# Optimization experiments

Measured on AMD Instinct MI355X. Metric: run time of the kernel, lower is better.

The kernel has to match this reference:

```python
import jax, jax.numpy as jnp
import numpy as np

B, H = 65536, 512


def setup_inputs() -> dict:
    key = jax.random.key(0)
    ks = jax.random.split(key, 10)
    s = 1.0 / np.sqrt(H)  # torch nn.Linear default init range
    uni = lambda k, shape: jax.random.uniform(k, shape, jnp.float32, -s, s)
    return {
        "inputs": jax.random.normal(ks[0], (B, H), jnp.float32),
        "short_term_memory": jax.random.normal(ks[1], (B, H), jnp.float32),
        "Wf": uni(ks[2], (H, H)), "bf": uni(ks[3], (H,)),
        "Wi": uni(ks[4], (H, H)), "bi": uni(ks[5], (H,)),
        "Wg": uni(ks[6], (H, H)), "bg": uni(ks[7], (H,)),
        "Wo": uni(ks[8], (H, H)), "bo": uni(ks[9], (H,)),
    }


def reference(inputs, short_term_memory, Wf, bf, Wi, bi, Wg, bg, Wo, bo):
    z = inputs + short_term_memory  # [B, H]
    # ForgetGate: OVERWRITES long-term memory (previous cell state never read).
    c = jax.nn.sigmoid(z @ Wf.T + bf)
    # InputGate: c += sigmoid(...) * tanh(...)
    c = c + jax.nn.sigmoid(z @ Wi.T + bi) * jnp.tanh(z @ Wg.T + bg)
    # OutputGate: h = tanh(c) * sigmoid(...)
    h = jnp.tanh(c) * jax.nn.sigmoid(z @ Wo.T + bo)
    return jnp.stack((c, h))  # [2, B, H]: new long-term and short-term memory
```

## Files before the change

### kernel.cpp

```cpp
#include <hip/hip_runtime.h>

typedef __bf16 bf16x8 __attribute__((ext_vector_type(8)));
typedef float  f32x4  __attribute__((ext_vector_type(4)));

#define LOG2E 1.4426950408889634f

static __device__ __forceinline__ float fexp2(float x) { return __builtin_amdgcn_exp2f(x); }
static __device__ __forceinline__ float frcp(float x)  { return __builtin_amdgcn_rcpf(x); }
static __device__ __forceinline__ float fsigmoid(float x) { return frcp(1.0f + fexp2(-LOG2E * x)); }
static __device__ __forceinline__ float ftanh(float x)    { return 2.0f * frcp(1.0f + fexp2(-2.0f * LOG2E * x)) - 1.0f; }

__global__ __launch_bounds__(256) void wpack(const float* __restrict__ Wf,
                                             const float* __restrict__ Wi,
                                             const float* __restrict__ Wg,
                                             const float* __restrict__ Wo,
                                             __bf16* __restrict__ Wp)
{
    int idx = blockIdx.x * 256 + threadIdx.x;
    int kg  = idx & 63;
    int j   = (idx >> 6) & 511;
    int g   = idx >> 15;
    const float* src = (g == 0) ? Wf : (g == 1) ? Wi : (g == 2) ? Wg : Wo;
    const float4* s4 = (const float4*)(src + j * 512 + kg * 8);
    float4 v0 = s4[0], v1 = s4[1];
    bf16x8 o;
    o[0] = (__bf16)v0.x; o[1] = (__bf16)v0.y; o[2] = (__bf16)v0.z; o[3] = (__bf16)v0.w;
    o[4] = (__bf16)v1.x; o[5] = (__bf16)v1.y; o[6] = (__bf16)v1.z; o[7] = (__bf16)v1.w;
    int cn = j >> 4;
    int ks = kg >> 2;
    int lt = (j & 15) + (kg & 3) * 16;
    size_t dst = ((size_t)(((g * 32 + cn) * 16 + ks) * 64 + lt)) * 8;
    *(bf16x8*)(Wp + dst) = o;
}

__global__ __launch_bounds__(1024, 4) void lstm_main(
    const float* __restrict__ xin, const float* __restrict__ stm,
    const __bf16* __restrict__ Wp,
    const float* __restrict__ bfv, const float* __restrict__ biv,
    const float* __restrict__ bgv, const float* __restrict__ bov,
    float* __restrict__ out)
{
    __shared__ unsigned char zs[131072];
    const int tid  = threadIdx.x;
    const int lane = tid & 63;
    const int wv   = tid >> 6;
    const int cn8  = wv & 7;
    const int rh   = wv >> 3;
    const int l15  = lane & 15;
    const int lq   = lane >> 4;
    const int row0 = blockIdx.x * 128;

    {
        const float* xb = xin + (size_t)row0 * 512;
        const float* sb = stm + (size_t)row0 * 512;
        #pragma unroll
        for (int it = 0; it < 8; ++it) {
            int idx = it * 1024 + tid;
            int row = idx >> 6;
            int kg  = idx & 63;
            const float4* x4 = (const float4*)(xb + row * 512 + kg * 8);
            const float4* s4 = (const float4*)(sb + row * 512 + kg * 8);
            float4 a0 = x4[0], a1 = x4[1];
            float4 b0 = s4[0], b1 = s4[1];
            bf16x8 p;
            p[0] = (__bf16)(a0.x + b0.x); p[1] = (__bf16)(a0.y + b0.y);
            p[2] = (__bf16)(a0.z + b0.z); p[3] = (__bf16)(a0.w + b0.w);
            p[4] = (__bf16)(a1.x + b1.x); p[5] = (__bf16)(a1.y + b1.y);
            p[6] = (__bf16)(a1.z + b1.z); p[7] = (__bf16)(a1.w + b1.w);
            int rb   = row >> 5;
            int kk   = kg >> 1;
            int slot = ((row & 31) + (kg & 1) * 32) ^ (kk & 7);
            *(bf16x8*)(zs + rb * 32768 + kk * 1024 + slot * 16) = p;
        }
    }
    __syncthreads();

    const int kkoff = lq >> 1;
    const int s0    = l15 + (lq & 1) * 32;
    const int koffb = kkoff << 10;
    const int abase = rh * 65536;

    for (int ci = 0; ci < 4; ++ci) {
        const int cn   = ci * 8 + cn8;
        const int colj = cn * 16 + l15;

        const __bf16* bp0 = Wp + ((size_t)((  0 + cn) * 16)) * 512 + lane * 8;
        const __bf16* bp1 = Wp + ((size_t)(( 32 + cn) * 16)) * 512 + lane * 8;
        const __bf16* bp2 = Wp + ((size_t)(( 64 + cn) * 16)) * 512 + lane * 8;
        const __bf16* bp3 = Wp + ((size_t)(( 96 + cn) * 16)) * 512 + lane * 8;

        float bias0 = bfv[colj], bias1 = biv[colj], bias2 = bgv[colj], bias3 = bov[colj];
        f32x4 acc[4][4];
        #pragma unroll
        for (int m = 0; m < 4; ++m) {
            #pragma unroll
            for (int r = 0; r < 4; ++r) {
                acc[m][0][r] = bias0; acc[m][1][r] = bias1;
                acc[m][2][r] = bias2; acc[m][3][r] = bias3;
            }
        }

        #pragma unroll 2
        for (int ks = 0; ks < 16; ++ks) {
            const int kk7 = ((2 * ks) & 7) | kkoff;
            const int t0  = abase + ((s0 ^ kk7) << 4) + ks * 2048 + koffb;
            bf16x8 b0 = *(const bf16x8*)(bp0 + ks * 512);
            bf16x8 b1 = *(const bf16x8*)(bp1 + ks * 512);
            bf16x8 b2 = *(const bf16x8*)(bp2 + ks * 512);
            bf16x8 b3 = *(const bf16x8*)(bp3 + ks * 512);
            bf16x8 a[4];
            #pragma unroll
            for (int m = 0; m < 4; ++m)
                a[m] = *(const bf16x8*)(zs + (m >> 1) * 32768 + (m & 1) * 256 + t0);
            #pragma unroll
            for (int m = 0; m < 4; ++m) {
                acc[m][0] = __builtin_amdgcn_mfma_f32_16x16x32_bf16(a[m], b0, acc[m][0], 0, 0, 0);
                acc[m][1] = __builtin_amdgcn_mfma_f32_16x16x32_bf16(a[m], b1, acc[m][1], 0, 0, 0);
                acc[m][2] = __builtin_amdgcn_mfma_f32_16x16x32_bf16(a[m], b2, acc[m][2], 0, 0, 0);
                acc[m][3] = __builtin_amdgcn_mfma_f32_16x16x32_bf16(a[m], b3, acc[m][3], 0, 0, 0);
            }
        }

        #pragma unroll
        for (int m = 0; m < 4; ++m) {
            #pragma unroll
            for (int r = 0; r < 4; ++r) {
                float F = acc[m][0][r], I = acc[m][1][r];
                float G = acc[m][2][r], O = acc[m][3][r];
                float c = fsigmoid(F) + fsigmoid(I) * ftanh(G);
                float h = ftanh(c) * fsigmoid(O);
                int row = row0 + rh * 64 + m * 16 + lq * 4 + r;
                int o   = row * 512 + colj;
                out[o] = c;
                out[33554432 + o] = h;
            }
        }
    }
}

extern "C" void kernel_launch(void* const* d_in, const int* in_sizes, int n_in,
                              void* d_out, int out_size, void* d_ws, size_t ws_size,
                              hipStream_t stream) {
    const float* xin = (const float*)d_in[0];
    const float* stm = (const float*)d_in[1];
    const float* Wf  = (const float*)d_in[2];
    const float* bf_ = (const float*)d_in[3];
    const float* Wi  = (const float*)d_in[4];
    const float* bi_ = (const float*)d_in[5];
    const float* Wg  = (const float*)d_in[6];
    const float* bg_ = (const float*)d_in[7];
    const float* Wo  = (const float*)d_in[8];
    const float* bo_ = (const float*)d_in[9];
    __bf16* Wp = (__bf16*)d_ws;

    wpack<<<512, 256, 0, stream>>>(Wf, Wi, Wg, Wo, Wp);
    lstm_main<<<512, 1024, 0, stream>>>(xin, stm, Wp, bf_, bi_, bg_, bo_, (float*)d_out);
}
```

Measured before the change: 202.7 us.

## Split gates across wave halves and exchange accumulators through LDS

Each wave now computes two gates for all 128 rows of the block instead of all four gates for 64 rows. Each weight fragment loaded from global memory is therefore reused across 8 row tiles rather than 4, halving B-operand traffic per wave. The cost is doubled A-operand LDS reads per wave, a 32 KB LDS exchange buffer, and extra __syncthreads in the epilogue to swap partial gate results between the paired waves. The larger LDS footprint may also lower occupancy.

```diff
diff --git a/kernel.cpp b/kernel.cpp
--- a/kernel.cpp
+++ b/kernel.cpp
@@ -41,6 +41,7 @@
     float* __restrict__ out)
 {
     __shared__ unsigned char zs[131072];
+    __shared__ unsigned char xbuf[32768];
     const int tid  = threadIdx.x;
     const int lane = tid & 63;
     const int wv   = tid >> 6;
@@ -78,58 +79,66 @@
     const int kkoff = lq >> 1;
     const int s0    = l15 + (lq & 1) * 32;
     const int koffb = kkoff << 10;
-    const int abase = rh * 65536;
+
+    const float* bias_a = rh ? bgv : bfv;
+    const float* bias_b = rh ? bov : biv;
 
     for (int ci = 0; ci < 4; ++ci) {
         const int cn   = ci * 8 + cn8;
         const int colj = cn * 16 + l15;
 
-        const __bf16* bp0 = Wp + ((size_t)((  0 + cn) * 16)) * 512 + lane * 8;
-        const __bf16* bp1 = Wp + ((size_t)(( 32 + cn) * 16)) * 512 + lane * 8;
-        const __bf16* bp2 = Wp + ((size_t)(( 64 + cn) * 16)) * 512 + lane * 8;
-        const __bf16* bp3 = Wp + ((size_t)(( 96 + cn) * 16)) * 512 + lane * 8;
+        const __bf16* bpA = Wp + ((size_t)(((rh * 2    ) * 32 + cn) * 16)) * 512 + lane * 8;
+        const __bf16* bpB = Wp + ((size_t)(((rh * 2 + 1) * 32 + cn) * 16)) * 512 + lane * 8;
 
-        float bias0 = bfv[colj], bias1 = biv[colj], bias2 = bgv[colj], bias3 = bov[colj];
-        f32x4 acc[4][4];
+        float biasA = bias_a[colj], biasB = bias_b[colj];
+        f32x4 acc[8][2];
         #pragma unroll
-        for (int m = 0; m < 4; ++m) {
+        for (int m = 0; m < 8; ++m) {
             #pragma unroll
-            for (int r = 0; r < 4; ++r) {
-                acc[m][0][r] = bias0; acc[m][1][r] = bias1;
-                acc[m][2][r] = bias2; acc[m][3][r] = bias3;
-            }
+            for (int r = 0; r < 4; ++r) { acc[m][0][r] = biasA; acc[m][1][r] = biasB; }
         }
 
         #pragma unroll 2
         for (int ks = 0; ks < 16; ++ks) {
             const int kk7 = ((2 * ks) & 7) | kkoff;
-            const int t0  = abase + ((s0 ^ kk7) << 4) + ks * 2048 + koffb;
-            bf16x8 b0 = *(const bf16x8*)(bp0 + ks * 512);
-            bf16x8 b1 = *(const bf16x8*)(bp1 + ks * 512);
-            bf16x8 b2 = *(const bf16x8*)(bp2 + ks * 512);
-            bf16x8 b3 = *(const bf16x8*)(bp3 + ks * 512);
-            bf16x8 a[4];
+            const int t0  = ((s0 ^ kk7) << 4) + ks * 2048 + koffb;
+            bf16x8 b0 = *(const bf16x8*)(bpA + ks * 512);
+            bf16x8 b1 = *(const bf16x8*)(bpB + ks * 512);
+            bf16x8 a[8];
             #pragma unroll
-            for (int m = 0; m < 4; ++m)
+            for (int m = 0; m < 8; ++m)
                 a[m] = *(const bf16x8*)(zs + (m >> 1) * 32768 + (m & 1) * 256 + t0);
             #pragma unroll
-            for (int m = 0; m < 4; ++m) {
+            for (int m = 0; m < 8; ++m) {
                 acc[m][0] = __builtin_amdgcn_mfma_f32_16x16x32_bf16(a[m], b0, acc[m][0], 0, 0, 0);
                 acc[m][1] = __builtin_amdgcn_mfma_f32_16x16x32_bf16(a[m], b1, acc[m][1], 0, 0, 0);
-                acc[m][2] = __builtin_amdgcn_mfma_f32_16x16x32_bf16(a[m], b2, acc[m][2], 0, 0, 0);
-                acc[m][3] = __builtin_amdgcn_mfma_f32_16x16x32_bf16(a[m], b3, acc[m][3], 0, 0, 0);
             }
         }
 
+        unsigned char* wr = xbuf + ((cn8 * 2 + rh) * 2) * 1024 + lane * 16;
+        unsigned char* rd = xbuf + ((cn8 * 2 + (1 - rh)) * 2) * 1024 + lane * 16;
         #pragma unroll
-        for (int m = 0; m < 4; ++m) {
+        for (int mc = 0; mc < 4; ++mc) {
+            __syncthreads();
+            if (rh == 0) {
+                *(f32x4*)(wr)        = acc[mc + 4][0];
+                *(f32x4*)(wr + 1024) = acc[mc + 4][1];
+            } else {
+                *(f32x4*)(wr)        = acc[mc][0];
+                *(f32x4*)(wr + 1024) = acc[mc][1];
+            }
+            __syncthreads();
+            f32x4 t0v = *(const f32x4*)(rd);
+            f32x4 t1v = *(const f32x4*)(rd + 1024);
+            int mo = rh ? (mc + 4) : mc;
             #pragma unroll
             for (int r = 0; r < 4; ++r) {
-                float F = acc[m][0][r], I = acc[m][1][r];
-                float G = acc[m][2][r], O = acc[m][3][r];
+                float F, I, G, O;
+                if (rh == 0) { F = acc[mc][0][r];     I = acc[mc][1][r];     G = t0v[r]; O = t1v[r]; }
+                else         { F = t0v[r]; I = t1v[r]; G = acc[mc + 4][0][r]; O = acc[mc + 4][1][r]; }
                 float c = fsigmoid(F) + fsigmoid(I) * ftanh(G);
                 float h = ftanh(c) * fsigmoid(O);
-                int row = row0 + rh * 64 + m * 16 + lq * 4 + r;
+                int row = row0 + mo * 16 + lq * 4 + r;
                 int o   = row * 512 + colj;
                 out[o] = c;
                 out[33554432 + o] = h;
```

New measurement: 219.8 us. 1.08x slower.

## Make LSTM kernel persistent with double-buffered z tiles and gate-interleaved weights

Applied to the files above, without the earlier changes.

The main kernel becomes persistent: 256 blocks of 512 threads each process four 64-row tiles. While MFMAs run on the current tile, the next tile's inputs are loaded and summed into a second LDS buffer. Weights are repacked so the four gates for a k-step sit next to each other, letting one base pointer fetch all four B fragments. This aims to hide global-load latency behind compute, at the cost of fewer waves per CU, more register pressure from the prefetch registers, and a grid that no longer matches a one-block-per-tile launch.

```diff
diff --git a/kernel.cpp b/kernel.cpp
--- a/kernel.cpp
+++ b/kernel.cpp
@@ -29,11 +29,11 @@
     int cn = j >> 4;
     int ks = kg >> 2;
     int lt = (j & 15) + (kg & 3) * 16;
-    size_t dst = ((size_t)(((g * 32 + cn) * 16 + ks) * 64 + lt)) * 8;
+    size_t dst = ((size_t)(((cn * 16 + ks) * 4 + g) * 64 + lt)) * 8;
     *(bf16x8*)(Wp + dst) = o;
 }
 
-__global__ __launch_bounds__(1024, 4) void lstm_main(
+__global__ __launch_bounds__(512, 2) void lstm_main(
     const float* __restrict__ xin, const float* __restrict__ stm,
     const __bf16* __restrict__ Wp,
     const float* __restrict__ bfv, const float* __restrict__ biv,
@@ -44,98 +44,125 @@
     const int tid  = threadIdx.x;
     const int lane = tid & 63;
     const int wv   = tid >> 6;
-    const int cn8  = wv & 7;
-    const int rh   = wv >> 3;
     const int l15  = lane & 15;
     const int lq   = lane >> 4;
-    const int row0 = blockIdx.x * 128;
+    const int b    = blockIdx.x;
+
+    const int kkoff = lq >> 1;
+    const int sl0   = l15 + (lq & 1) * 32;
+    const int koffb = kkoff << 10;
+
+    const int st_kk   = lane >> 1;
+    const int st_hi   = (lane & 1) << 5;
+    const int st_xor  = st_kk & 7;
+    const int st_base = st_kk << 10;
+
+#define STLOAD(X0, X1, S0, S1, RND, ROWB) { \
+    const float* xp_ = xin + ((ROWB) + (RND) * 8 + wv) * 512 + lane * 8; \
+    const float* sp_ = stm + ((ROWB) + (RND) * 8 + wv) * 512 + lane * 8; \
+    X0 = *(const float4*)(xp_);     X1 = *(const float4*)(xp_ + 4); \
+    S0 = *(const float4*)(sp_);     S1 = *(const float4*)(sp_ + 4); }
+
+#define STWRITE(X0, X1, S0, S1, RND, BUF) { \
+    bf16x8 p_; \
+    p_[0] = (__bf16)(X0.x + S0.x); p_[1] = (__bf16)(X0.y + S0.y); \
+    p_[2] = (__bf16)(X0.z + S0.z); p_[3] = (__bf16)(X0.w + S0.w); \
+    p_[4] = (__bf16)(X1.x + S1.x); p_[5] = (__bf16)(X1.y + S1.y); \
+    p_[6] = (__bf16)(X1.z + S1.z); p_[7] = (__bf16)(X1.w + S1.w); \
+    int row_ = (RND) * 8 + wv; \
+    int byte_ = ((row_ >> 5) << 15) | st_base | \
+                (((((row_ & 31) + st_hi)) ^ st_xor) << 4); \
+    *(bf16x8*)((BUF) + byte_) = p_; }
+
+    unsigned char* bufc = zs;
+    unsigned char* bufn = zs + 65536;
 
     {
-        const float* xb = xin + (size_t)row0 * 512;
-        const float* sb = stm + (size_t)row0 * 512;
+        const size_t prow = (size_t)b * 64;
         #pragma unroll
-        for (int it = 0; it < 8; ++it) {
-            int idx = it * 1024 + tid;
-            int row = idx >> 6;
-            int kg  = idx & 63;
-            const float4* x4 = (const float4*)(xb + row * 512 + kg * 8);
-            const float4* s4 = (const float4*)(sb + row * 512 + kg * 8);
-            float4 a0 = x4[0], a1 = x4[1];
-            float4 b0 = s4[0], b1 = s4[1];
-            bf16x8 p;
-            p[0] = (__bf16)(a0.x + b0.x); p[1] = (__bf16)(a0.y + b0.y);
-            p[2] = (__bf16)(a0.z + b0.z); p[3] = (__bf16)(a0.w + b0.w);
-            p[4] = (__bf16)(a1.x + b1.x); p[5] = (__bf16)(a1.y + b1.y);
-            p[6] = (__bf16)(a1.z + b1.z); p[7] = (__bf16)(a1.w + b1.w);
-            int rb   = row >> 5;
-            int kk   = kg >> 1;
-            int slot = ((row & 31) + (kg & 1) * 32) ^ (kk & 7);
-            *(bf16x8*)(zs + rb * 32768 + kk * 1024 + slot * 16) = p;
+        for (int rnd = 0; rnd < 8; ++rnd) {
+            float4 x0, x1, s0v, s1v;
+            STLOAD(x0, x1, s0v, s1v, rnd, prow)
+            STWRITE(x0, x1, s0v, s1v, rnd, bufc)
         }
     }
     __syncthreads();
 
-    const int kkoff = lq >> 1;
-    const int s0    = l15 + (lq & 1) * 32;
-    const int koffb = kkoff << 10;
-    const int abase = rh * 65536;
+    for (int t = 0; t < 4; ++t) {
+        const int tile = b + t * 256;
+        const int row0 = tile * 64;
+        const bool stg = (t < 3);
+        const size_t nrow = (size_t)(tile + 256) * 64;
 
-    for (int ci = 0; ci < 4; ++ci) {
-        const int cn   = ci * 8 + cn8;
-        const int colj = cn * 16 + l15;
+        for (int ci = 0; ci < 4; ++ci) {
+            const int cn   = ci * 8 + wv;
+            const int colj = cn * 16 + l15;
+            const __bf16* bp = Wp + (size_t)cn * 32768 + lane * 8;
 
-        const __bf16* bp0 = Wp + ((size_t)((  0 + cn) * 16)) * 512 + lane * 8;
-        const __bf16* bp1 = Wp + ((size_t)(( 32 + cn) * 16)) * 512 + lane * 8;
-        const __bf16* bp2 = Wp + ((size_t)(( 64 + cn) * 16)) * 512 + lane * 8;
-        const __bf16* bp3 = Wp + ((size_t)(( 96 + cn) * 16)) * 512 + lane * 8;
+            float bias0 = bfv[colj], bias1 = biv[colj];
+            float bias2 = bgv[colj], bias3 = bov[colj];
+            f32x4 acc[4][4];
+            #pragma unroll
+            for (int m = 0; m < 4; ++m) {
+                #pragma unroll
+                for (int r = 0; r < 4; ++r) {
+                    acc[m][0][r] = bias0; acc[m][1][r] = bias1;
+                    acc[m][2][r] = bias2; acc[m][3][r] = bias3;
+                }
+            }
 
-        float bias0 = bfv[colj], bias1 = biv[colj], bias2 = bgv[colj], bias3 = bov[colj];
-        f32x4 acc[4][4];
-        #pragma unroll
-        for (int m = 0; m < 4; ++m) {
+            float4 ax0, ax1, as0, as1;
+            float4 bx0, bx1, bs0, bs1;
+
             #pragma unroll
-            for (int r = 0; r < 4; ++r) {
-                acc[m][0][r] = bias0; acc[m][1][r] = bias1;
-                acc[m][2][r] = bias2; acc[m][3][r] = bias3;
+            for (int ks = 0; ks < 16; ++ks) {
+                if (stg) {
+                    if (ks == 0) STLOAD(ax0, ax1, as0, as1, 2 * ci,     nrow)
+                    if (ks == 1) STLOAD(bx0, bx1, bs0, bs1, 2 * ci + 1, nrow)
+                    if (ks == 8) STWRITE(ax0, ax1, as0, as1, 2 * ci,     bufn)
+                    if (ks == 9) STWRITE(bx0, bx1, bs0, bs1, 2 * ci + 1, bufn)
+                }
+                const int kk7 = ((2 * ks) & 7) | kkoff;
+                const int t0  = ((sl0 ^ kk7) << 4) + ks * 2048 + koffb;
+                const __bf16* p_ = bp + ks * 2048;
+                bf16x8 b0 = *(const bf16x8*)(p_);
+                bf16x8 b1 = *(const bf16x8*)(p_ + 512);
+                bf16x8 b2 = *(const bf16x8*)(p_ + 1024);
+                bf16x8 b3 = *(const bf16x8*)(p_ + 1536);
+                bf16x8 a[4];
+                #pragma unroll
+                for (int m = 0; m < 4; ++m)
+                    a[m] = *(const bf16x8*)(bufc + (m >> 1) * 32768 + (m & 1) * 256 + t0);
+                #pragma unroll
+                for (int m = 0; m < 4; ++m) {
+                    acc[m][0] = __builtin_amdgcn_mfma_f32_16x16x32_bf16(a[m], b0, acc[m][0], 0, 0, 0);
+                    acc[m][1] = __builtin_amdgcn_mfma_f32_16x16x32_bf16(a[m], b1, acc[m][1], 0, 0, 0);
+                    acc[m][2] = __builtin_amdgcn_mfma_f32_16x16x32_bf16(a[m], b2, acc[m][2], 0, 0, 0);
+                    acc[m][3] = __builtin_amdgcn_mfma_f32_16x16x32_bf16(a[m], b3, acc[m][3], 0, 0, 0);
+                }
+            }
+
+            #pragma unroll
+            for (int m = 0; m < 4; ++m) {
+                #pragma unroll
+                for (int r = 0; r < 4; ++r) {
+                    float F = acc[m][0][r], I = acc[m][1][r];
+                    float G = acc[m][2][r], O = acc[m][3][r];
+                    float c = fsigmoid(F) + fsigmoid(I) * ftanh(G);
+                    float h = ftanh(c) * fsigmoid(O);
+                    int row = row0 + m * 16 + lq * 4 + r;
+                    int o   = row * 512 + colj;
+                    out[o] = c;
+                    out[33554432 + o] = h;
+                }
             }
         }
 
-        #pragma unroll 2
-        for (int ks = 0; ks < 16; ++ks) {
-            const int kk7 = ((2 * ks) & 7) | kkoff;
-            const int t0  = abase + ((s0 ^ kk7) << 4) + ks * 2048 + koffb;
-            bf16x8 b0 = *(const bf16x8*)(bp0 + ks * 512);
-            bf16x8 b1 = *(const bf16x8*)(bp1 + ks * 512);
-            bf16x8 b2 = *(const bf16x8*)(bp2 + ks * 512);
-            bf16x8 b3 = *(const bf16x8*)(bp3 + ks * 512);
-            bf16x8 a[4];
-            #pragma unroll
-            for (int m = 0; m < 4; ++m)
-                a[m] = *(const bf16x8*)(zs + (m >> 1) * 32768 + (m & 1) * 256 + t0);
-            #pragma unroll
-            for (int m = 0; m < 4; ++m) {
-                acc[m][0] = __builtin_amdgcn_mfma_f32_16x16x32_bf16(a[m], b0, acc[m][0], 0, 0, 0);
-                acc[m][1] = __builtin_amdgcn_mfma_f32_16x16x32_bf16(a[m], b1, acc[m][1], 0, 0, 0);
-                acc[m][2] = __builtin_amdgcn_mfma_f32_16x16x32_bf16(a[m], b2, acc[m][2], 0, 0, 0);
-                acc[m][3] = __builtin_amdgcn_mfma_f32_16x16x32_bf16(a[m], b3, acc[m][3], 0, 0, 0);
-            }
-        }
-
-        #pragma unroll
-        for (int m = 0; m < 4; ++m) {
-            #pragma unroll
-            for (int r = 0; r < 4; ++r) {
-                float F = acc[m][0][r], I = acc[m][1][r];
-                float G = acc[m][2][r], O = acc[m][3][r];
-                float c = fsigmoid(F) + fsigmoid(I) * ftanh(G);
-                float h = ftanh(c) * fsigmoid(O);
-                int row = row0 + rh * 64 + m * 16 + lq * 4 + r;
-                int o   = row * 512 + colj;
-                out[o] = c;
-                out[33554432 + o] = h;
-            }
-        }
+        __syncthreads();
+        unsigned char* tmp = bufc; bufc = bufn; bufn = tmp;
     }
+#undef STLOAD
+#undef STWRITE
 }
 
 extern "C" void kernel_launch(void* const* d_in, const int* in_sizes, int n_in,
@@ -154,5 +181,5 @@
     __bf16* Wp = (__bf16*)d_ws;
 
     wpack<<<512, 256, 0, stream>>>(Wf, Wi, Wg, Wo, Wp);
-    lstm_main<<<512, 1024, 0, stream>>>(xin, stm, Wp, bf_, bi_, bg_, bo_, (float*)d_out);
+    lstm_main<<<256, 512, 0, stream>>>(xin, stm, Wp, bf_, bi_, bg_, bo_, (float*)d_out);
 }
```

After: 215.8 us. +6.4%, slower.
